# Optimization experiments

Measured on AMD Instinct MI355X. Metric: run time of the kernel, lower is better.

Reference implementation:

```python
import jax, jax.numpy as jnp
import numpy as np

B, D, H, NC = 4096, 128, 4, 10
HD = D // H
EPS = 1e-5


def _ln(x, g, b):
    m = jnp.mean(x, axis=-1, keepdims=True)
    v = jnp.var(x, axis=-1, keepdims=True)
    return (x - m) * jax.lax.rsqrt(v + EPS) * g + b


def _mlp(x, w1, b1, w2, b2):
    h = jax.nn.gelu(x @ w1.T + b1, approximate=False)  # nn.GELU default = exact erf
    return h @ w2.T + b2


def setup_inputs():
    key = jax.random.key(0)
    ks = iter(jax.random.split(key, 40))
    w = lambda *s: jax.random.normal(next(ks), s, dtype=jnp.float32) * 0.02
    inp = {
        'coords': jax.random.uniform(next(ks), (B, 2), dtype=jnp.float32),
        'labels': jax.random.randint(next(ks), (B,), 0, NC),
        'ce_w': w(D, 2), 'ce_b': w(D),
        'emb': w(NC, D),
        'sa_in_w': w(3 * D, D), 'sa_in_b': w(3 * D),
        'sa_out_w': w(D, D), 'sa_out_b': w(D),
        'n1_g': jnp.ones(D), 'n1_b': jnp.zeros(D),
        'm1_w1': w(4 * D, D), 'm1_b1': w(4 * D), 'm1_w2': w(D, 4 * D), 'm1_b2': w(D),
        'n2_g': jnp.ones(D), 'n2_b': jnp.zeros(D),
        'ca_in_w': w(3 * D, D), 'ca_in_b': w(3 * D),
        'ca_out_w': w(D, D), 'ca_out_b': w(D),
        'n3_g': jnp.ones(D), 'n3_b': jnp.zeros(D),
        'm2_w1': w(4 * D, D), 'm2_b1': w(4 * D), 'm2_w2': w(D, 4 * D), 'm2_b2': w(D),
        'n4_g': jnp.ones(D), 'n4_b': jnp.zeros(D),
        'fin_w': w(1, D), 'fin_b': w(1),
    }
    return inp


def reference(coords, labels, ce_w, ce_b, emb, sa_in_w, sa_in_b, sa_out_w, sa_out_b,
              n1_g, n1_b, m1_w1, m1_b1, m1_w2, m1_b2, n2_g, n2_b,
              ca_in_w, ca_in_b, ca_out_w, ca_out_b, n3_g, n3_b,
              m2_w1, m2_b1, m2_w2, m2_b2, n4_g, n4_b, fin_w, fin_b):
    # --- vectorized positional encoding (original loops over batch) ---
    div = 10000.0 ** (2.0 * jnp.arange(D // 2, dtype=jnp.float32) / D)  # [D/2]
    pe_sin = jnp.sin(coords[:, 0:1] / div)  # even slots
    pe_cos = jnp.cos(coords[:, 1:2] / div)  # odd slots
    pe = jnp.stack([pe_sin, pe_cos], axis=-1).reshape(B, D)

    x = coords @ ce_w.T + ce_b + pe  # [B, D]

    # --- self-attention: seq_len = B, batch = 1 (torch seq-first semantics) ---
    qkv = x @ sa_in_w.T + sa_in_b  # [B, 3D]
    q, k, v = jnp.split(qkv, 3, axis=-1)
    q = q.reshape(B, H, HD); k = k.reshape(B, H, HD); v = v.reshape(B, H, HD)
    scores = jnp.einsum('qhd,khd->hqk', q, k) / jnp.sqrt(jnp.float32(HD))  # [H,B,B]
    attn = jax.nn.softmax(scores, axis=-1)
    sa = jnp.einsum('hqk,khd->qhd', attn, v).reshape(B, D) @ sa_out_w.T + sa_out_b

    x = _ln(x + sa, n1_g, n1_b)
    x = _ln(x + _mlp(x, m1_w1, m1_b1, m1_w2, m1_b2), n2_g, n2_b)

    # --- cross-attention: per-sample q_len = kv_len = 1 -> softmax over a
    # single key is exactly 1, so output = out_proj(v_proj(label_emb)) ---
    lab = emb[labels]  # [B, D]
    wv = ca_in_w[2 * D:]; bv = ca_in_b[2 * D:]
    ca = (lab @ wv.T + bv) @ ca_out_w.T + ca_out_b

    x = _ln(x + ca, n3_g, n3_b)
    x = _ln(x + _mlp(x, m2_w1, m2_b1, m2_w2, m2_b2), n4_g, n4_b)

    return jax.nn.sigmoid(x @ fin_w.T + fin_b)  # [B, 1]
```

## Files before the change

### kernel.cpp

```cpp
#include <hip/hip_runtime.h>
#include <hip/hip_bf16.h>


typedef __bf16 bf16_t;
typedef __bf16 bf16x8 __attribute__((ext_vector_type(8)));
typedef __bf16 bf16x4 __attribute__((ext_vector_type(4)));
typedef __bf16 bf16x2 __attribute__((ext_vector_type(2)));
typedef float  f32x4  __attribute__((ext_vector_type(4)));
typedef float  f32x2  __attribute__((ext_vector_type(2)));

__device__ __forceinline__ f32x4 mfma16(bf16x8 a, bf16x8 b, f32x4 c) {
  return __builtin_amdgcn_mfma_f32_16x16x32_bf16(a, b, c, 0, 0, 0);
}

__global__ __launch_bounds__(256) void k_init(const float* __restrict__ coords,
                                              const float* __restrict__ ce_w,
                                              const float* __restrict__ ce_b,
                                              float* __restrict__ xf,
                                              bf16_t* __restrict__ xb,
                                              const float* __restrict__ s0,
                                              const float* __restrict__ s1,
                                              const float* __restrict__ s2,
                                              const float* __restrict__ s3,
                                              const float* __restrict__ s4,
                                              const float* __restrict__ s5,
                                              bf16_t* __restrict__ wdst,
                                              const float* __restrict__ emb,
                                              const float* __restrict__ wvp,
                                              const float* __restrict__ bvp,
                                              const float* __restrict__ cow,
                                              const float* __restrict__ cob,
                                              float* __restrict__ tab) {
  const int bid = blockIdx.x;
  const int tid = threadIdx.x;
  if (bid < 2048) {
    int row = bid * 2 + (tid >> 7);
    int d   = tid & 127;
    float c0 = coords[row * 2 + 0];
    float c1 = coords[row * 2 + 1];
    int   j  = d >> 1;
    float inv = exp2f(-0.20762050593045953f * (float)j);
    float pe  = (d & 1) ? cosf(c1 * inv) : sinf(c0 * inv);
    float x = c0 * ce_w[2 * d] + c1 * ce_w[2 * d + 1] + ce_b[d] + pe;
    xf[(size_t)row * 128 + d] = x;
    xb[(size_t)row * 128 + d] = (bf16_t)x;
  } else if (bid < 2368) {
    int i = (bid - 2048) * 256 + tid;
    const float* src; int off;
    if      (i < 12288) { src = s0; off = i; }
    else if (i < 16384) { src = s1; off = i - 12288; }
    else if (i < 32768) { src = s2; off = i - 16384; }
    else if (i < 49152) { src = s3; off = i - 32768; }
    else if (i < 65536) { src = s4; off = i - 49152; }
    else                { src = s5; off = i - 65536; }
    f32x4 v = *(const f32x4*)(src + (size_t)off * 4);
    bf16x4 o = {(bf16_t)v[0], (bf16_t)v[1], (bf16_t)v[2], (bf16_t)v[3]};
    *(bf16x4*)(wdst + (size_t)i * 4) = o;
  } else {
    __shared__ float embs[10][128];
    __shared__ float t1[10][128];
    for (int i = tid; i < 1280; i += 256) embs[i >> 7][i & 127] = emb[i];
    __syncthreads();
    for (int o = tid; o < 1280; o += 256) {
      int c = o >> 7, n = o & 127;
      float acc = bvp[n];
      const float* wr = wvp + n * 128;
      for (int k2 = 0; k2 < 128; k2++) acc += embs[c][k2] * wr[k2];
      t1[c][n] = acc;
    }
    __syncthreads();
    for (int o = tid; o < 1280; o += 256) {
      int c = o >> 7, dd = o & 127;
      float acc = cob[dd];
      const float* wr = cow + dd * 128;
      for (int n = 0; n < 128; n++) acc += t1[c][n] * wr[n];
      tab[o] = acc;
    }
  }
}

enum { EPI_BF16 = 1, EPI_GELU_BF16 = 2 };

template <int K, int EPI>
__global__ __launch_bounds__(256) void k_gemm(const bf16_t* __restrict__ X,
                                              const bf16_t* __restrict__ Wb,
                                              const float* __restrict__ bias,
                                              bf16_t* __restrict__ outB,
                                              bf16_t* __restrict__ vTout,
                                              int N) {
  const int tid  = threadIdx.x;
  const int lane = tid & 63;
  const int wv   = tid >> 6;
  const int l15  = lane & 15;
  const int quad = lane >> 4;
  const int xbase = blockIdx.x * 64 + (wv >> 1) * 32;
  const int wbase = blockIdx.y * 64 + (wv & 1) * 32;

  const bf16_t* wr0 = Wb + (size_t)(wbase + l15) * K + quad * 8;
  const bf16_t* xr0 = X  + (size_t)(xbase + l15) * K + quad * 8;

  f32x4 acc[2][2];
  const f32x4 zero4 = {0.f, 0.f, 0.f, 0.f};
  for (int i = 0; i < 2; i++)
    for (int t = 0; t < 2; t++) acc[i][t] = zero4;

#pragma unroll 4
  for (int kk = 0; kk < K; kk += 32) {
    bf16x8 a0 = *(const bf16x8*)(wr0 + kk);
    bf16x8 a1 = *(const bf16x8*)(wr0 + 16 * K + kk);
    bf16x8 b0 = *(const bf16x8*)(xr0 + kk);
    bf16x8 b1 = *(const bf16x8*)(xr0 + 16 * K + kk);
    acc[0][0] = mfma16(a0, b0, acc[0][0]);
    acc[0][1] = mfma16(a0, b1, acc[0][1]);
    acc[1][0] = mfma16(a1, b0, acc[1][0]);
    acc[1][1] = mfma16(a1, b1, acc[1][1]);
  }

  f32x4 bv[2];
  bv[0] = *(const f32x4*)(bias + wbase + quad * 4);
  bv[1] = *(const f32x4*)(bias + wbase + 16 + quad * 4);
#pragma unroll
  for (int t = 0; t < 2; t++) {
    int row = xbase + t * 16 + l15;
#pragma unroll
    for (int i = 0; i < 2; i++) {
      int col0 = wbase + i * 16 + quad * 4;
      f32x4 v = acc[i][t] + bv[i];
      if (EPI == EPI_GELU_BF16) {
#pragma unroll
        for (int r = 0; r < 4; r++)
          v[r] = 0.5f * v[r] * (1.0f + erff(v[r] * 0.70710678118654752f));
      }
      bf16x4 o = {(bf16_t)v[0], (bf16_t)v[1], (bf16_t)v[2], (bf16_t)v[3]};
      *(bf16x4*)(outB + (size_t)row * N + col0) = o;
      if (vTout && col0 >= 256) {
#pragma unroll
        for (int r = 0; r < 4; r++)
          vTout[(size_t)(col0 - 256 + r) * 4096 + row] = (bf16_t)v[r];
      }
    }
  }
}

__global__ __launch_bounds__(256, 4) void k_attn(const bf16_t* __restrict__ qkv,
                                                 const bf16_t* __restrict__ vT,
                                                 bf16_t* __restrict__ opart,
                                                 float* __restrict__ lpart) {
  __shared__ bf16_t kbuf[128][36];
  __shared__ bf16_t vbuf[32][136];
  __shared__ bf16_t pt[4][2][16][72];

  const int tid  = threadIdx.x;
  const int lane = tid & 63;
  const int wv   = tid >> 6;
  const int l15  = lane & 15;
  const int quad = lane >> 4;
  const int blk  = blockIdx.x;
  const int h    = blk & 3;
  const int ks   = (blk >> 2) & 7;
  const int qt   = (blk >> 5) * 4 + wv;
  const int q0   = qt * 32;
  const int kb   = ks * 512;
  const int task = (qt * 8 + ks) * 4 + h;

  bf16x8 qfA, qfB;
  {
    bf16x8 ra = *(const bf16x8*)(qkv + (size_t)(q0 + l15) * 384 + h * 32 + quad * 8);
    bf16x8 rb = *(const bf16x8*)(qkv + (size_t)(q0 + 16 + l15) * 384 + h * 32 + quad * 8);
#pragma unroll
    for (int j = 0; j < 8; j++) {
      qfA[j] = (bf16_t)((float)ra[j] * 0.17677669529663687f);
      qfB[j] = (bf16_t)((float)rb[j] * 0.17677669529663687f);
    }
  }

  const f32x4 zero4 = {0.f, 0.f, 0.f, 0.f};
  f32x4 oA0 = zero4, oA1 = zero4, oB0 = zero4, oB1 = zero4;
  float laccA = 0.f, laccB = 0.f;

  for (int kk = 0; kk < 512; kk += 128) {
    __syncthreads();
#pragma unroll
    for (int rep = 0; rep < 2; rep++) {
      int idx = rep * 256 + tid;
      int row = idx >> 2, seg = idx & 3;
      bf16x8 t8 = *(const bf16x8*)(qkv + (size_t)(kb + kk + row) * 384
                                   + 128 + h * 32 + seg * 8);
      *(bf16x8*)&kbuf[row][seg * 8] = t8;
      int dim = idx >> 4, vseg = idx & 15;
      bf16x8 v8 = *(const bf16x8*)(vT + (size_t)(h * 32 + dim) * 4096
                                   + kb + kk + vseg * 8);
      *(bf16x8*)&vbuf[dim][vseg * 8] = v8;
    }
    __syncthreads();

#pragma unroll
    for (int half = 0; half < 2; half++) {
      const int ko = half * 64;
      bf16x8 kf0 = *(const bf16x8*)&kbuf[ko + l15][quad * 8];
      bf16x8 kf1 = *(const bf16x8*)&kbuf[ko + 16 + l15][quad * 8];
      bf16x8 kf2 = *(const bf16x8*)&kbuf[ko + 32 + l15][quad * 8];
      bf16x8 kf3 = *(const bf16x8*)&kbuf[ko + 48 + l15][quad * 8];

      f32x4 sA[4], sB[4];
      sA[0] = mfma16(kf0, qfA, zero4);
      sA[1] = mfma16(kf1, qfA, zero4);
      sA[2] = mfma16(kf2, qfA, zero4);
      sA[3] = mfma16(kf3, qfA, zero4);
      sB[0] = mfma16(kf0, qfB, zero4);
      sB[1] = mfma16(kf1, qfB, zero4);
      sB[2] = mfma16(kf2, qfB, zero4);
      sB[3] = mfma16(kf3, qfB, zero4);

#pragma unroll
      for (int t = 0; t < 4; t++) {
        float a0 = __expf(sA[t][0]), a1 = __expf(sA[t][1]);
        float a2 = __expf(sA[t][2]), a3 = __expf(sA[t][3]);
        laccA += (a0 + a1) + (a2 + a3);
        bf16x4 pa = {(bf16_t)a0, (bf16_t)a1, (bf16_t)a2, (bf16_t)a3};
        *(bf16x4*)&pt[wv][0][l15][t * 16 + quad * 4] = pa;
        float b0 = __expf(sB[t][0]), b1 = __expf(sB[t][1]);
        float b2 = __expf(sB[t][2]), b3 = __expf(sB[t][3]);
        laccB += (b0 + b1) + (b2 + b3);
        bf16x4 pb = {(bf16_t)b0, (bf16_t)b1, (bf16_t)b2, (bf16_t)b3};
        *(bf16x4*)&pt[wv][1][l15][t * 16 + quad * 4] = pb;
      }

      bf16x8 pA0 = *(const bf16x8*)&pt[wv][0][l15][quad * 8];
      bf16x8 pA1 = *(const bf16x8*)&pt[wv][0][l15][32 + quad * 8];
      bf16x8 pB0 = *(const bf16x8*)&pt[wv][1][l15][quad * 8];
      bf16x8 pB1 = *(const bf16x8*)&pt[wv][1][l15][32 + quad * 8];

      bf16x8 v00 = *(const bf16x8*)&vbuf[l15][ko + quad * 8];
      bf16x8 v01 = *(const bf16x8*)&vbuf[16 + l15][ko + quad * 8];
      bf16x8 v10 = *(const bf16x8*)&vbuf[l15][ko + 32 + quad * 8];
      bf16x8 v11 = *(const bf16x8*)&vbuf[16 + l15][ko + 32 + quad * 8];

      oA0 = mfma16(pA0, v00, oA0);
      oA0 = mfma16(pA1, v10, oA0);
      oA1 = mfma16(pA0, v01, oA1);
      oA1 = mfma16(pA1, v11, oA1);
      oB0 = mfma16(pB0, v00, oB0);
      oB0 = mfma16(pB1, v10, oB0);
      oB1 = mfma16(pB0, v01, oB1);
      oB1 = mfma16(pB1, v11, oB1);
    }
  }

  laccA += __shfl_xor(laccA, 16, 64); laccA += __shfl_xor(laccA, 32, 64);
  laccB += __shfl_xor(laccB, 16, 64); laccB += __shfl_xor(laccB, 32, 64);
  if (quad == 0) {
    lpart[task * 32 + l15]      = laccA;
    lpart[task * 32 + 16 + l15] = laccB;
  }

  size_t ob = (size_t)task * 1024;
#pragma unroll
  for (int r = 0; r < 4; r++) {
    int qa = quad * 4 + r;
    opart[ob + qa * 32 + l15]             = (bf16_t)oA0[r];
    opart[ob + qa * 32 + 16 + l15]        = (bf16_t)oA1[r];
    opart[ob + (16 + qa) * 32 + l15]      = (bf16_t)oB0[r];
    opart[ob + (16 + qa) * 32 + 16 + l15] = (bf16_t)oB1[r];
  }
}

__global__ __launch_bounds__(256) void k_attn_fin(const bf16_t* __restrict__ opart,
                                                  const float* __restrict__ lpart,
                                                  bf16_t* __restrict__ attnb) {
  int idx = blockIdx.x * 256 + threadIdx.x;
  int d  = idx & 31;
  int q  = (idx >> 5) & 4095;
  int h  = idx >> 17;
  int qt = q >> 5, ql = q & 31;
  float O = 0.f, L = 0.f;
#pragma unroll
  for (int ks = 0; ks < 8; ks++) {
    int t = (qt * 8 + ks) * 4 + h;
    O += (float)opart[(size_t)t * 1024 + ql * 32 + d];
    L += lpart[t * 32 + ql];
  }
  attnb[(size_t)q * 128 + h * 32 + d] = (bf16_t)(O / L);
}

__global__ __launch_bounds__(512) void k_tail(
    const bf16_t* __restrict__ attnb, const float* __restrict__ xf,
    const bf16_t* __restrict__ wso, const float* __restrict__ bso,
    const float* __restrict__ n1g, const float* __restrict__ n1b,
    const bf16_t* __restrict__ w11, const float* __restrict__ b11,
    const bf16_t* __restrict__ w12, const float* __restrict__ b12,
    const float* __restrict__ n2g, const float* __restrict__ n2b,
    const int* __restrict__ labels, const float* __restrict__ tab,
    const float* __restrict__ n3g, const float* __restrict__ n3b,
    const bf16_t* __restrict__ w21, const float* __restrict__ b21,
    const bf16_t* __restrict__ w22, const float* __restrict__ b22,
    const float* __restrict__ n4g, const float* __restrict__ n4b,
    const float* __restrict__ fw, const float* __restrict__ fb,
    float* __restrict__ out) {
  __shared__ float  xs[16][132];
  __shared__ bf16_t xsb[16][136];
  __shared__ bf16_t hb[16][520];
  __shared__ float  red[2][16][8];

  const int tid  = threadIdx.x;
  const int lane = tid & 63;
  const int wv   = tid >> 6;
  const int l15  = lane & 15;
  const int quad = lane >> 4;
  const int row  = blockIdx.x * 16 + l15;
  const int cb1  = wv * 16;
  const int c1   = cb1 + quad * 4;
  const int cb4  = wv * 64;

  const f32x4 zero4 = {0.f, 0.f, 0.f, 0.f};

  {
    f32x4 acc = zero4;
    const bf16_t* br = attnb + (size_t)row * 128 + quad * 8;
    const bf16_t* ar = wso + (size_t)(cb1 + l15) * 128 + quad * 8;
#pragma unroll
    for (int kk = 0; kk < 128; kk += 32)
      acc = mfma16(*(const bf16x8*)(ar + kk), *(const bf16x8*)(br + kk), acc);

    f32x4 v = acc + *(const f32x4*)(bso + c1)
                  + *(const f32x4*)(xf + (size_t)row * 128 + c1);
    float s  = (v[0] + v[1]) + (v[2] + v[3]);
    float sq = (v[0]*v[0] + v[1]*v[1]) + (v[2]*v[2] + v[3]*v[3]);
    s  += __shfl_xor(s, 16, 64);  s  += __shfl_xor(s, 32, 64);
    sq += __shfl_xor(sq, 16, 64); sq += __shfl_xor(sq, 32, 64);
    if (quad == 0) { red[0][l15][wv] = s; red[1][l15][wv] = sq; }
    __syncthreads();
    float S = 0.f, SQ = 0.f;
#pragma unroll
    for (int w2 = 0; w2 < 8; w2++) { S += red[0][l15][w2]; SQ += red[1][l15][w2]; }
    float mean = S * (1.f / 128.f);
    float rstd = rsqrtf(SQ * (1.f / 128.f) - mean * mean + 1e-5f);
    f32x4 y = (v - mean) * rstd * (*(const f32x4*)(n1g + c1))
            + *(const f32x4*)(n1b + c1);
    *(f32x4*)&xs[l15][c1] = y;
    bf16x4 o = {(bf16_t)y[0], (bf16_t)y[1], (bf16_t)y[2], (bf16_t)y[3]};
    *(bf16x4*)&xsb[l15][c1] = o;
  }
  __syncthreads();

  {
    f32x4 au[4] = {zero4, zero4, zero4, zero4};
#pragma unroll
    for (int kk = 0; kk < 128; kk += 32) {
      bf16x8 bfr = *(const bf16x8*)&xsb[l15][kk + quad * 8];
#pragma unroll
      for (int i = 0; i < 4; i++) {
        bf16x8 a = *(const bf16x8*)(w11 + (size_t)(cb4 + i * 16 + l15) * 128
                                    + kk + quad * 8);
        au[i] = mfma16(a, bfr, au[i]);
      }
    }
#pragma unroll
    for (int i = 0; i < 4; i++) {
      int c = cb4 + i * 16 + quad * 4;
      f32x4 vv = au[i] + *(const f32x4*)(b11 + c);
#pragma unroll
      for (int r = 0; r < 4; r++)
        vv[r] = 0.5f * vv[r] * (1.0f + erff(vv[r] * 0.70710678118654752f));
      bf16x4 o = {(bf16_t)vv[0], (bf16_t)vv[1], (bf16_t)vv[2], (bf16_t)vv[3]};
      *(bf16x4*)&hb[l15][c] = o;
    }
  }
  __syncthreads();

  {
    f32x4 acc = zero4;
    const bf16_t* ar = w12 + (size_t)(cb1 + l15) * 512 + quad * 8;
#pragma unroll 4
    for (int kk = 0; kk < 512; kk += 32) {
      bf16x8 bfr = *(const bf16x8*)&hb[l15][kk + quad * 8];
      acc = mfma16(*(const bf16x8*)(ar + kk), bfr, acc);
    }
    f32x4 v = acc + *(const f32x4*)(b12 + c1) + *(const f32x4*)&xs[l15][c1];
    float s  = (v[0] + v[1]) + (v[2] + v[3]);
    float sq = (v[0]*v[0] + v[1]*v[1]) + (v[2]*v[2] + v[3]*v[3]);
    s  += __shfl_xor(s, 16, 64);  s  += __shfl_xor(s, 32, 64);
    sq += __shfl_xor(sq, 16, 64); sq += __shfl_xor(sq, 32, 64);
    if (quad == 0) { red[0][l15][wv] = s; red[1][l15][wv] = sq; }
    __syncthreads();
    float S = 0.f, SQ = 0.f;
#pragma unroll
    for (int w2 = 0; w2 < 8; w2++) { S += red[0][l15][w2]; SQ += red[1][l15][w2]; }
    float mean = S * (1.f / 128.f);
    float rstd = rsqrtf(SQ * (1.f / 128.f) - mean * mean + 1e-5f);
    int lab = labels[row];
    f32x4 y = (v - mean) * rstd * (*(const f32x4*)(n2g + c1))
            + *(const f32x4*)(n2b + c1)
            + *(const f32x4*)(tab + (size_t)lab * 128 + c1);
    float s3  = (y[0] + y[1]) + (y[2] + y[3]);
    float sq3 = (y[0]*y[0] + y[1]*y[1]) + (y[2]*y[2] + y[3]*y[3]);
    s3  += __shfl_xor(s3, 16, 64);  s3  += __shfl_xor(s3, 32, 64);
    sq3 += __shfl_xor(sq3, 16, 64); sq3 += __shfl_xor(sq3, 32, 64);
    __syncthreads();
    if (quad == 0) { red[0][l15][wv] = s3; red[1][l15][wv] = sq3; }
    __syncthreads();
    float S3 = 0.f, SQ3 = 0.f;
#pragma unroll
    for (int w2 = 0; w2 < 8; w2++) { S3 += red[0][l15][w2]; SQ3 += red[1][l15][w2]; }
    float mean3 = S3 * (1.f / 128.f);
    float rstd3 = rsqrtf(SQ3 * (1.f / 128.f) - mean3 * mean3 + 1e-5f);
    f32x4 y3 = (y - mean3) * rstd3 * (*(const f32x4*)(n3g + c1))
             + *(const f32x4*)(n3b + c1);
    *(f32x4*)&xs[l15][c1] = y3;
    bf16x4 o = {(bf16_t)y3[0], (bf16_t)y3[1], (bf16_t)y3[2], (bf16_t)y3[3]};
    *(bf16x4*)&xsb[l15][c1] = o;
  }
  __syncthreads();

  {
    f32x4 au[4] = {zero4, zero4, zero4, zero4};
#pragma unroll
    for (int kk = 0; kk < 128; kk += 32) {
      bf16x8 bfr = *(const bf16x8*)&xsb[l15][kk + quad * 8];
#pragma unroll
      for (int i = 0; i < 4; i++) {
        bf16x8 a = *(const bf16x8*)(w21 + (size_t)(cb4 + i * 16 + l15) * 128
                                    + kk + quad * 8);
        au[i] = mfma16(a, bfr, au[i]);
      }
    }
#pragma unroll
    for (int i = 0; i < 4; i++) {
      int c = cb4 + i * 16 + quad * 4;
      f32x4 vv = au[i] + *(const f32x4*)(b21 + c);
#pragma unroll
      for (int r = 0; r < 4; r++)
        vv[r] = 0.5f * vv[r] * (1.0f + erff(vv[r] * 0.70710678118654752f));
      bf16x4 o = {(bf16_t)vv[0], (bf16_t)vv[1], (bf16_t)vv[2], (bf16_t)vv[3]};
      *(bf16x4*)&hb[l15][c] = o;
    }
  }
  __syncthreads();

  {
    f32x4 acc = zero4;
    const bf16_t* ar = w22 + (size_t)(cb1 + l15) * 512 + quad * 8;
#pragma unroll 4
    for (int kk = 0; kk < 512; kk += 32) {
      bf16x8 bfr = *(const bf16x8*)&hb[l15][kk + quad * 8];
      acc = mfma16(*(const bf16x8*)(ar + kk), bfr, acc);
    }
    f32x4 v = acc + *(const f32x4*)(b22 + c1) + *(const f32x4*)&xs[l15][c1];
    float s  = (v[0] + v[1]) + (v[2] + v[3]);
    float sq = (v[0]*v[0] + v[1]*v[1]) + (v[2]*v[2] + v[3]*v[3]);
    s  += __shfl_xor(s, 16, 64);  s  += __shfl_xor(s, 32, 64);
    sq += __shfl_xor(sq, 16, 64); sq += __shfl_xor(sq, 32, 64);
    if (quad == 0) { red[0][l15][wv] = s; red[1][l15][wv] = sq; }
    __syncthreads();
    float S = 0.f, SQ = 0.f;
#pragma unroll
    for (int w2 = 0; w2 < 8; w2++) { S += red[0][l15][w2]; SQ += red[1][l15][w2]; }
    float mean = S * (1.f / 128.f);
    float rstd = rsqrtf(SQ * (1.f / 128.f) - mean * mean + 1e-5f);
    f32x4 y = (v - mean) * rstd * (*(const f32x4*)(n4g + c1))
            + *(const f32x4*)(n4b + c1);
    f32x4 fwv = *(const f32x4*)(fw + c1);
    float dot = (y[0]*fwv[0] + y[1]*fwv[1]) + (y[2]*fwv[2] + y[3]*fwv[3]);
    dot += __shfl_xor(dot, 16, 64); dot += __shfl_xor(dot, 32, 64);
    __syncthreads();
    if (quad == 0) red[0][l15][wv] = dot;
    __syncthreads();
    if (wv == 0 && quad == 0) {
      float logit = fb[0];
#pragma unroll
      for (int w2 = 0; w2 < 8; w2++) logit += red[0][l15][w2];
      out[row] = 1.0f / (1.0f + expf(-logit));
    }
  }
}

extern "C" void kernel_launch(void* const* d_in, const int* in_sizes, int n_in,
                              void* d_out, int out_size, void* d_ws, size_t ws_size,
                              hipStream_t stream) {
  const float* coords  = (const float*)d_in[0];
  const int*   labels  = (const int*)d_in[1];
  const float* ce_w    = (const float*)d_in[2];
  const float* ce_b    = (const float*)d_in[3];
  const float* emb     = (const float*)d_in[4];
  const float* sa_in_w = (const float*)d_in[5];
  const float* sa_in_b = (const float*)d_in[6];
  const float* sa_out_w= (const float*)d_in[7];
  const float* sa_out_b= (const float*)d_in[8];
  const float* n1_g    = (const float*)d_in[9];
  const float* n1_b    = (const float*)d_in[10];
  const float* m1_w1   = (const float*)d_in[11];
  const float* m1_b1   = (const float*)d_in[12];
  const float* m1_w2   = (const float*)d_in[13];
  const float* m1_b2   = (const float*)d_in[14];
  const float* n2_g    = (const float*)d_in[15];
  const float* n2_b    = (const float*)d_in[16];
  const float* ca_in_w = (const float*)d_in[17];
  const float* ca_in_b = (const float*)d_in[18];
  const float* ca_out_w= (const float*)d_in[19];
  const float* ca_out_b= (const float*)d_in[20];
  const float* n3_g    = (const float*)d_in[21];
  const float* n3_b    = (const float*)d_in[22];
  const float* m2_w1   = (const float*)d_in[23];
  const float* m2_b1   = (const float*)d_in[24];
  const float* m2_w2   = (const float*)d_in[25];
  const float* m2_b2   = (const float*)d_in[26];
  const float* n4_g    = (const float*)d_in[27];
  const float* n4_b    = (const float*)d_in[28];
  const float* fin_w   = (const float*)d_in[29];
  const float* fin_b   = (const float*)d_in[30];
  float* outp = (float*)d_out;

  char* w = (char*)d_ws;
  float*  xf    = (float*)(w);
  float*  tab   = (float*)(w + 2097152);
  bf16_t* wsb   = (bf16_t*)(w + 2105344);
  bf16_t* xb    = (bf16_t*)(w + 2760704);
  bf16_t* attnb = (bf16_t*)(w + 3809280);
  bf16_t* qkvb  = (bf16_t*)(w + 4857856);
  bf16_t* vT    = (bf16_t*)(w + 8003584);
  bf16_t* opart = (bf16_t*)(w + 9052160);
  float*  lpart = (float*)(w + 17440768);

  bf16_t* w_sain  = wsb;
  bf16_t* w_saout = wsb + 49152;
  bf16_t* w_m1w1  = wsb + 65536;
  bf16_t* w_m1w2  = wsb + 131072;
  bf16_t* w_m2w1  = wsb + 196608;
  bf16_t* w_m2w2  = wsb + 262144;

  k_init<<<2369, 256, 0, stream>>>(coords, ce_w, ce_b, xf, xb,
                                   sa_in_w, sa_out_w, m1_w1, m1_w2, m2_w1, m2_w2,
                                   wsb, emb, ca_in_w + 256 * 128, ca_in_b + 256,
                                   ca_out_w, ca_out_b, tab);
  k_gemm<128, EPI_BF16><<<dim3(64, 6), 256, 0, stream>>>(xb, w_sain, sa_in_b,
                                                         qkvb, vT, 384);
  k_attn<<<1024, 256, 0, stream>>>(qkvb, vT, opart, lpart);
  k_attn_fin<<<2048, 256, 0, stream>>>(opart, lpart, attnb);
  k_tail<<<256, 512, 0, stream>>>(attnb, xf,
                                  w_saout, sa_out_b, n1_g, n1_b,
                                  w_m1w1, m1_b1, w_m1w2, m1_b2, n2_g, n2_b,
                                  labels, tab, n3_g, n3_b,
                                  w_m2w1, m2_b1, w_m2w2, m2_b2, n4_g, n4_b,
                                  fin_w, fin_b, outp);

  (void)in_sizes; (void)n_in; (void)out_size; (void)ws_size;
}
```

Baseline: 192.6 us.

## Fuse all stages into one cooperative persistent kernel with grid syncs

Merges the init, QKV GEMM, attention, attention-finalize and tail kernels into a single cooperative kernel of 256 blocks x 512 threads, separated by grid.sync barriers. The attention-finalize step now runs inside the tail phase, so the bf16 attention output no longer goes through global memory. The aim is to remove launch overheads and inter-kernel gaps. In exchange, attention runs on far fewer resident waves (two task iterations per 4-wave group instead of 1024 independent blocks), which may lower latency hiding, and each grid-wide barrier adds its own cost.

```diff
diff --git a/kernel.cpp b/kernel.cpp
--- a/kernel.cpp
+++ b/kernel.cpp
@@ -1,475 +1,470 @@
 #include <hip/hip_runtime.h>
 #include <hip/hip_bf16.h>
-
+#include <hip/hip_cooperative_groups.h>
+
+
+namespace cg = cooperative_groups;
 
 typedef __bf16 bf16_t;
 typedef __bf16 bf16x8 __attribute__((ext_vector_type(8)));
 typedef __bf16 bf16x4 __attribute__((ext_vector_type(4)));
-typedef __bf16 bf16x2 __attribute__((ext_vector_type(2)));
 typedef float  f32x4  __attribute__((ext_vector_type(4)));
-typedef float  f32x2  __attribute__((ext_vector_type(2)));
 
 __device__ __forceinline__ f32x4 mfma16(bf16x8 a, bf16x8 b, f32x4 c) {
   return __builtin_amdgcn_mfma_f32_16x16x32_bf16(a, b, c, 0, 0, 0);
 }
 
-__global__ __launch_bounds__(256) void k_init(const float* __restrict__ coords,
-                                              const float* __restrict__ ce_w,
-                                              const float* __restrict__ ce_b,
-                                              float* __restrict__ xf,
-                                              bf16_t* __restrict__ xb,
-                                              const float* __restrict__ s0,
-                                              const float* __restrict__ s1,
-                                              const float* __restrict__ s2,
-                                              const float* __restrict__ s3,
-                                              const float* __restrict__ s4,
-                                              const float* __restrict__ s5,
-                                              bf16_t* __restrict__ wdst,
-                                              const float* __restrict__ emb,
-                                              const float* __restrict__ wvp,
-                                              const float* __restrict__ bvp,
-                                              const float* __restrict__ cow,
-                                              const float* __restrict__ cob,
-                                              float* __restrict__ tab) {
-  const int bid = blockIdx.x;
-  const int tid = threadIdx.x;
-  if (bid < 2048) {
-    int row = bid * 2 + (tid >> 7);
-    int d   = tid & 127;
-    float c0 = coords[row * 2 + 0];
-    float c1 = coords[row * 2 + 1];
-    int   j  = d >> 1;
-    float inv = exp2f(-0.20762050593045953f * (float)j);
-    float pe  = (d & 1) ? cosf(c1 * inv) : sinf(c0 * inv);
-    float x = c0 * ce_w[2 * d] + c1 * ce_w[2 * d + 1] + ce_b[d] + pe;
-    xf[(size_t)row * 128 + d] = x;
-    xb[(size_t)row * 128 + d] = (bf16_t)x;
-  } else if (bid < 2368) {
-    int i = (bid - 2048) * 256 + tid;
-    const float* src; int off;
-    if      (i < 12288) { src = s0; off = i; }
-    else if (i < 16384) { src = s1; off = i - 12288; }
-    else if (i < 32768) { src = s2; off = i - 16384; }
-    else if (i < 49152) { src = s3; off = i - 32768; }
-    else if (i < 65536) { src = s4; off = i - 49152; }
-    else                { src = s5; off = i - 65536; }
-    f32x4 v = *(const f32x4*)(src + (size_t)off * 4);
-    bf16x4 o = {(bf16_t)v[0], (bf16_t)v[1], (bf16_t)v[2], (bf16_t)v[3]};
-    *(bf16x4*)(wdst + (size_t)i * 4) = o;
-  } else {
-    __shared__ float embs[10][128];
-    __shared__ float t1[10][128];
-    for (int i = tid; i < 1280; i += 256) embs[i >> 7][i & 127] = emb[i];
-    __syncthreads();
-    for (int o = tid; o < 1280; o += 256) {
-      int c = o >> 7, n = o & 127;
-      float acc = bvp[n];
-      const float* wr = wvp + n * 128;
-      for (int k2 = 0; k2 < 128; k2++) acc += embs[c][k2] * wr[k2];
-      t1[c][n] = acc;
-    }
-    __syncthreads();
-    for (int o = tid; o < 1280; o += 256) {
-      int c = o >> 7, dd = o & 127;
-      float acc = cob[dd];
-      const float* wr = cow + dd * 128;
-      for (int n = 0; n < 128; n++) acc += t1[c][n] * wr[n];
-      tab[o] = acc;
-    }
-  }
-}
-
-enum { EPI_BF16 = 1, EPI_GELU_BF16 = 2 };
-
-template <int K, int EPI>
-__global__ __launch_bounds__(256) void k_gemm(const bf16_t* __restrict__ X,
-                                              const bf16_t* __restrict__ Wb,
-                                              const float* __restrict__ bias,
-                                              bf16_t* __restrict__ outB,
-                                              bf16_t* __restrict__ vTout,
-                                              int N) {
+struct P {
+  const float* coords; const int* labels;
+  const float* ce_w;   const float* ce_b;
+  const float* sa_in_b; const float* sa_out_b;
+  const float* n1g; const float* n1b;
+  const float* m1_b1; const float* m1_b2;
+  const float* n2g; const float* n2b;
+  const float* n3g; const float* n3b;
+  const float* m2_b1; const float* m2_b2;
+  const float* n4g; const float* n4b;
+  const float* fin_w; const float* fin_b;
+  const float* s0; const float* s1; const float* s2;
+  const float* s3; const float* s4; const float* s5;
+  const float* emb; const float* wvp; const float* bvp;
+  const float* cow; const float* cob;
+  float* xf; float* tab; bf16_t* wsb; bf16_t* xb;
+  bf16_t* qkvb; bf16_t* vT; bf16_t* opart; float* lpart;
+  const bf16_t* w_sain; const bf16_t* w_saout;
+  const bf16_t* w_m1w1; const bf16_t* w_m1w2;
+  const bf16_t* w_m2w1; const bf16_t* w_m2w2;
+  float* out;
+};
+
+#define SM_KBUF(g)  ((g) * 9216)
+#define SM_VBUF(g)  (18432 + (g) * 8704)
+#define SM_PT(wv)   (35840 + (wv) * 4608)
+
+__global__ __launch_bounds__(512, 2) void k_fused(P p) {
+  cg::grid_group grid = cg::this_grid();
+  __shared__ char smem[74240] __attribute__((aligned(16)));
+
+  const int b    = blockIdx.x;
   const int tid  = threadIdx.x;
   const int lane = tid & 63;
   const int wv   = tid >> 6;
   const int l15  = lane & 15;
   const int quad = lane >> 4;
-  const int xbase = blockIdx.x * 64 + (wv >> 1) * 32;
-  const int wbase = blockIdx.y * 64 + (wv & 1) * 32;
-
-  const bf16_t* wr0 = Wb + (size_t)(wbase + l15) * K + quad * 8;
-  const bf16_t* xr0 = X  + (size_t)(xbase + l15) * K + quad * 8;
-
-  f32x4 acc[2][2];
   const f32x4 zero4 = {0.f, 0.f, 0.f, 0.f};
-  for (int i = 0; i < 2; i++)
-    for (int t = 0; t < 2; t++) acc[i][t] = zero4;
-
+
+  {
+    int c = b * 512 + tid;
+    int row = c >> 5, d0 = (c & 31) * 4;
+    float c0 = p.coords[row * 2 + 0];
+    float c1 = p.coords[row * 2 + 1];
+    f32x4 xv; bf16x4 xo;
+#pragma unroll
+    for (int r = 0; r < 4; r++) {
+      int d = d0 + r, j = d >> 1;
+      float inv = exp2f(-0.20762050593045953f * (float)j);
+      float pe  = (d & 1) ? cosf(c1 * inv) : sinf(c0 * inv);
+      float x = c0 * p.ce_w[2 * d] + c1 * p.ce_w[2 * d + 1] + p.ce_b[d] + pe;
+      xv[r] = x; xo[r] = (bf16_t)x;
+    }
+    *(f32x4*)(p.xf + (size_t)row * 128 + d0) = xv;
+    *(bf16x4*)(p.xb + (size_t)row * 128 + d0) = xo;
+
+    if (c < 81920) {
+      const float* src; int off;
+      if      (c < 12288) { src = p.s0; off = c; }
+      else if (c < 16384) { src = p.s1; off = c - 12288; }
+      else if (c < 32768) { src = p.s2; off = c - 16384; }
+      else if (c < 49152) { src = p.s3; off = c - 32768; }
+      else if (c < 65536) { src = p.s4; off = c - 49152; }
+      else                { src = p.s5; off = c - 65536; }
+      f32x4 v = *(const f32x4*)(src + (size_t)off * 4);
+      bf16x4 o = {(bf16_t)v[0], (bf16_t)v[1], (bf16_t)v[2], (bf16_t)v[3]};
+      *(bf16x4*)(p.wsb + (size_t)c * 4) = o;
+    }
+
+    if (b == 255) {
+      float (*embs)[128] = (float(*)[128])smem;
+      float (*t1)[128]   = (float(*)[128])(smem + 5120);
+      for (int i = tid; i < 1280; i += 512) embs[i >> 7][i & 127] = p.emb[i];
+      __syncthreads();
+      for (int o = tid; o < 1280; o += 512) {
+        int cc = o >> 7, n = o & 127;
+        float acc = p.bvp[n];
+        const float* wr = p.wvp + n * 128;
+        for (int k2 = 0; k2 < 128; k2++) acc += embs[cc][k2] * wr[k2];
+        t1[cc][n] = acc;
+      }
+      __syncthreads();
+      for (int o = tid; o < 1280; o += 512) {
+        int cc = o >> 7, dd = o & 127;
+        float acc = p.cob[dd];
+        const float* wr = p.cow + dd * 128;
+        for (int n = 0; n < 128; n++) acc += t1[cc][n] * wr[n];
+        p.tab[o] = acc;
+      }
+    }
+  }
+  __threadfence();
+  grid.sync();
+
+  {
+    int W = b * 8 + wv;
+    if (W < 1536) {
+      int rt = W / 12, ct = W - rt * 12;
+      int row0 = rt * 32, col0 = ct * 32;
+      const bf16_t* wr0 = p.w_sain + (size_t)(col0 + l15) * 128 + quad * 8;
+      const bf16_t* xr0 = p.xb + (size_t)(row0 + l15) * 128 + quad * 8;
+      f32x4 acc[2][2];
+      for (int i = 0; i < 2; i++)
+        for (int t = 0; t < 2; t++) acc[i][t] = zero4;
+#pragma unroll
+      for (int kk = 0; kk < 128; kk += 32) {
+        bf16x8 a0 = *(const bf16x8*)(wr0 + kk);
+        bf16x8 a1 = *(const bf16x8*)(wr0 + 16 * 128 + kk);
+        bf16x8 b0 = *(const bf16x8*)(xr0 + kk);
+        bf16x8 b1 = *(const bf16x8*)(xr0 + 16 * 128 + kk);
+        acc[0][0] = mfma16(a0, b0, acc[0][0]);
+        acc[0][1] = mfma16(a0, b1, acc[0][1]);
+        acc[1][0] = mfma16(a1, b0, acc[1][0]);
+        acc[1][1] = mfma16(a1, b1, acc[1][1]);
+      }
+      f32x4 bv[2];
+      bv[0] = *(const f32x4*)(p.sa_in_b + col0 + quad * 4);
+      bv[1] = *(const f32x4*)(p.sa_in_b + col0 + 16 + quad * 4);
+#pragma unroll
+      for (int t = 0; t < 2; t++) {
+        int row = row0 + t * 16 + l15;
+#pragma unroll
+        for (int i = 0; i < 2; i++) {
+          int colb = col0 + i * 16 + quad * 4;
+          f32x4 v = acc[i][t] + bv[i];
+          bf16x4 o = {(bf16_t)v[0], (bf16_t)v[1], (bf16_t)v[2], (bf16_t)v[3]};
+          *(bf16x4*)(p.qkvb + (size_t)row * 384 + colb) = o;
+          if (colb >= 256) {
+#pragma unroll
+            for (int r = 0; r < 4; r++)
+              p.vT[(size_t)(colb - 256 + r) * 4096 + row] = (bf16_t)v[r];
+          }
+        }
+      }
+    }
+  }
+  __threadfence();
+  grid.sync();
+
+  {
+    const int g    = wv >> 2;
+    const int wl   = wv & 3;
+    const int gtid = wl * 64 + lane;
+    bf16_t (*kbuf)[36]      = (bf16_t(*)[36])(smem + SM_KBUF(g));
+    bf16_t (*vbuf)[136]     = (bf16_t(*)[136])(smem + SM_VBUF(g));
+    bf16_t (*ptw)[16][72]   = (bf16_t(*)[16][72])(smem + SM_PT(wv));
+
+    for (int j = 0; j < 2; j++) {
+      int orig = b * 4 + g * 2 + j;
+      int h  = orig & 3;
+      int ks = (orig >> 2) & 7;
+      int qt = (orig >> 5) * 4 + wl;
+      int q0 = qt * 32;
+      int kb = ks * 512;
+      int task = (qt * 8 + ks) * 4 + h;
+
+      bf16x8 qfA, qfB;
+      {
+        bf16x8 ra = *(const bf16x8*)(p.qkvb + (size_t)(q0 + l15) * 384 + h * 32 + quad * 8);
+        bf16x8 rb = *(const bf16x8*)(p.qkvb + (size_t)(q0 + 16 + l15) * 384 + h * 32 + quad * 8);
+#pragma unroll
+        for (int jj = 0; jj < 8; jj++) {
+          qfA[jj] = (bf16_t)((float)ra[jj] * 0.17677669529663687f);
+          qfB[jj] = (bf16_t)((float)rb[jj] * 0.17677669529663687f);
+        }
+      }
+
+      f32x4 oA0 = zero4, oA1 = zero4, oB0 = zero4, oB1 = zero4;
+      float laccA = 0.f, laccB = 0.f;
+
+      for (int kk = 0; kk < 512; kk += 128) {
+        __syncthreads();
+#pragma unroll
+        for (int rep = 0; rep < 2; rep++) {
+          int idx = rep * 256 + gtid;
+          int krow = idx >> 2, seg = idx & 3;
+          bf16x8 t8 = *(const bf16x8*)(p.qkvb + (size_t)(kb + kk + krow) * 384
+                                       + 128 + h * 32 + seg * 8);
+          *(bf16x8*)&kbuf[krow][seg * 8] = t8;
+          int dim = idx >> 4, vseg = idx & 15;
+          bf16x8 v8 = *(const bf16x8*)(p.vT + (size_t)(h * 32 + dim) * 4096
+                                       + kb + kk + vseg * 8);
+          *(bf16x8*)&vbuf[dim][vseg * 8] = v8;
+        }
+        __syncthreads();
+
+#pragma unroll
+        for (int half = 0; half < 2; half++) {
+          const int ko = half * 64;
+          bf16x8 kf0 = *(const bf16x8*)&kbuf[ko + l15][quad * 8];
+          bf16x8 kf1 = *(const bf16x8*)&kbuf[ko + 16 + l15][quad * 8];
+          bf16x8 kf2 = *(const bf16x8*)&kbuf[ko + 32 + l15][quad * 8];
+          bf16x8 kf3 = *(const bf16x8*)&kbuf[ko + 48 + l15][quad * 8];
+
+          f32x4 sA[4], sB[4];
+          sA[0] = mfma16(kf0, qfA, zero4);
+          sA[1] = mfma16(kf1, qfA, zero4);
+          sA[2] = mfma16(kf2, qfA, zero4);
+          sA[3] = mfma16(kf3, qfA, zero4);
+          sB[0] = mfma16(kf0, qfB, zero4);
+          sB[1] = mfma16(kf1, qfB, zero4);
+          sB[2] = mfma16(kf2, qfB, zero4);
+          sB[3] = mfma16(kf3, qfB, zero4);
+
+#pragma unroll
+          for (int t = 0; t < 4; t++) {
+            float a0 = __expf(sA[t][0]), a1 = __expf(sA[t][1]);
+            float a2 = __expf(sA[t][2]), a3 = __expf(sA[t][3]);
+            laccA += (a0 + a1) + (a2 + a3);
+            bf16x4 pa = {(bf16_t)a0, (bf16_t)a1, (bf16_t)a2, (bf16_t)a3};
+            *(bf16x4*)&ptw[0][l15][t * 16 + quad * 4] = pa;
+            float b0 = __expf(sB[t][0]), b1 = __expf(sB[t][1]);
+            float b2 = __expf(sB[t][2]), b3 = __expf(sB[t][3]);
+            laccB += (b0 + b1) + (b2 + b3);
+            bf16x4 pb = {(bf16_t)b0, (bf16_t)b1, (bf16_t)b2, (bf16_t)b3};
+            *(bf16x4*)&ptw[1][l15][t * 16 + quad * 4] = pb;
+          }
+
+          bf16x8 pA0 = *(const bf16x8*)&ptw[0][l15][quad * 8];
+          bf16x8 pA1 = *(const bf16x8*)&ptw[0][l15][32 + quad * 8];
+          bf16x8 pB0 = *(const bf16x8*)&ptw[1][l15][quad * 8];
+          bf16x8 pB1 = *(const bf16x8*)&ptw[1][l15][32 + quad * 8];
+
+          bf16x8 v00 = *(const bf16x8*)&vbuf[l15][ko + quad * 8];
+          bf16x8 v01 = *(const bf16x8*)&vbuf[16 + l15][ko + quad * 8];
+          bf16x8 v10 = *(const bf16x8*)&vbuf[l15][ko + 32 + quad * 8];
+          bf16x8 v11 = *(const bf16x8*)&vbuf[16 + l15][ko + 32 + quad * 8];
+
+          oA0 = mfma16(pA0, v00, oA0);
+          oA0 = mfma16(pA1, v10, oA0);
+          oA1 = mfma16(pA0, v01, oA1);
+          oA1 = mfma16(pA1, v11, oA1);
+          oB0 = mfma16(pB0, v00, oB0);
+          oB0 = mfma16(pB1, v10, oB0);
+          oB1 = mfma16(pB0, v01, oB1);
+          oB1 = mfma16(pB1, v11, oB1);
+        }
+      }
+
+      laccA += __shfl_xor(laccA, 16, 64); laccA += __shfl_xor(laccA, 32, 64);
+      laccB += __shfl_xor(laccB, 16, 64); laccB += __shfl_xor(laccB, 32, 64);
+      if (quad == 0) {
+        p.lpart[task * 32 + l15]      = laccA;
+        p.lpart[task * 32 + 16 + l15] = laccB;
+      }
+      size_t ob = (size_t)task * 1024;
+#pragma unroll
+      for (int r = 0; r < 4; r++) {
+        int qa = quad * 4 + r;
+        p.opart[ob + qa * 32 + l15]             = (bf16_t)oA0[r];
+        p.opart[ob + qa * 32 + 16 + l15]        = (bf16_t)oA1[r];
+        p.opart[ob + (16 + qa) * 32 + l15]      = (bf16_t)oB0[r];
+        p.opart[ob + (16 + qa) * 32 + 16 + l15] = (bf16_t)oB1[r];
+      }
+    }
+  }
+  __threadfence();
+  grid.sync();
+
+  {
+    float  (*xs)[132]    = (float(*)[132])(smem);
+    bf16_t (*xsb)[136]   = (bf16_t(*)[136])(smem + 8448);
+    bf16_t (*att)[136]   = (bf16_t(*)[136])(smem + 12800);
+    bf16_t (*hb)[520]    = (bf16_t(*)[520])(smem + 17152);
+    float  (*red)[16][8] = (float(*)[16][8])(smem + 33792);
+    float  (*Ls)[4]      = (float(*)[4])(smem + 34816);
+
+    const int row = b * 16 + l15;
+    const int cb1 = wv * 16;
+    const int c1  = cb1 + quad * 4;
+    const int cb4 = wv * 64;
+
+    if (tid < 64) {
+      int rr = tid >> 2, hh = tid & 3;
+      int q = b * 16 + rr, qt = q >> 5, ql = q & 31;
+      float L = 0.f;
+#pragma unroll
+      for (int ks = 0; ks < 8; ks++) L += p.lpart[((qt * 8 + ks) * 4 + hh) * 32 + ql];
+      Ls[rr][hh] = L;
+    }
+    __syncthreads();
+#pragma unroll
+    for (int r = 0; r < 4; r++) {
+      int idx = r * 512 + tid;
+      int rr = idx >> 7, d = idx & 127, hh = d >> 5, dd = d & 31;
+      int q = b * 16 + rr, qt = q >> 5, ql = q & 31;
+      float O = 0.f;
+#pragma unroll
+      for (int ks = 0; ks < 8; ks++)
+        O += (float)p.opart[(size_t)((qt * 8 + ks) * 4 + hh) * 1024 + ql * 32 + dd];
+      att[rr][d] = (bf16_t)(O / Ls[rr][hh]);
+    }
+    __syncthreads();
+
+    {
+      f32x4 acc = zero4;
+      const bf16_t* ar = p.w_saout + (size_t)(cb1 + l15) * 128 + quad * 8;
+#pragma unroll
+      for (int kk = 0; kk < 128; kk += 32) {
+        bf16x8 bfr = *(const bf16x8*)&att[l15][kk + quad * 8];
+        acc = mfma16(*(const bf16x8*)(ar + kk), bfr, acc);
+      }
+      f32x4 v = acc + *(const f32x4*)(p.sa_out_b + c1)
+                    + *(const f32x4*)(p.xf + (size_t)row * 128 + c1);
+      float s  = (v[0] + v[1]) + (v[2] + v[3]);
+      float sq = (v[0]*v[0] + v[1]*v[1]) + (v[2]*v[2] + v[3]*v[3]);
+      s  += __shfl_xor(s, 16, 64);  s  += __shfl_xor(s, 32, 64);
+      sq += __shfl_xor(sq, 16, 64); sq += __shfl_xor(sq, 32, 64);
+      if (quad == 0) { red[0][l15][wv] = s; red[1][l15][wv] = sq; }
+      __syncthreads();
+      float S = 0.f, SQ = 0.f;
+#pragma unroll
+      for (int w2 = 0; w2 < 8; w2++) { S += red[0][l15][w2]; SQ += red[1][l15][w2]; }
+      float mean = S * (1.f / 128.f);
+      float rstd = rsqrtf(SQ * (1.f / 128.f) - mean * mean + 1e-5f);
+      f32x4 y = (v - mean) * rstd * (*(const f32x4*)(p.n1g + c1))
+              + *(const f32x4*)(p.n1b + c1);
+      *(f32x4*)&xs[l15][c1] = y;
+      bf16x4 o = {(bf16_t)y[0], (bf16_t)y[1], (bf16_t)y[2], (bf16_t)y[3]};
+      *(bf16x4*)&xsb[l15][c1] = o;
+    }
+    __syncthreads();
+
+    {
+      f32x4 au[4] = {zero4, zero4, zero4, zero4};
+#pragma unroll
+      for (int kk = 0; kk < 128; kk += 32) {
+        bf16x8 bfr = *(const bf16x8*)&xsb[l15][kk + quad * 8];
+#pragma unroll
+        for (int i = 0; i < 4; i++) {
+          bf16x8 a = *(const bf16x8*)(p.w_m1w1 + (size_t)(cb4 + i * 16 + l15) * 128
+                                      + kk + quad * 8);
+          au[i] = mfma16(a, bfr, au[i]);
+        }
+      }
+#pragma unroll
+      for (int i = 0; i < 4; i++) {
+        int c = cb4 + i * 16 + quad * 4;
+        f32x4 vv = au[i] + *(const f32x4*)(p.m1_b1 + c);
+#pragma unroll
+        for (int r = 0; r < 4; r++)
+          vv[r] = 0.5f * vv[r] * (1.0f + erff(vv[r] * 0.70710678118654752f));
+        bf16x4 o = {(bf16_t)vv[0], (bf16_t)vv[1], (bf16_t)vv[2], (bf16_t)vv[3]};
+        *(bf16x4*)&hb[l15][c] = o;
+      }
+    }
+    __syncthreads();
+
+    {
+      f32x4 acc = zero4;
+      const bf16_t* ar = p.w_m1w2 + (size_t)(cb1 + l15) * 512 + quad * 8;
 #pragma unroll 4
-  for (int kk = 0; kk < K; kk += 32) {
-    bf16x8 a0 = *(const bf16x8*)(wr0 + kk);
-    bf16x8 a1 = *(const bf16x8*)(wr0 + 16 * K + kk);
-    bf16x8 b0 = *(const bf16x8*)(xr0 + kk);
-    bf16x8 b1 = *(const bf16x8*)(xr0 + 16 * K + kk);
-    acc[0][0] = mfma16(a0, b0, acc[0][0]);
-    acc[0][1] = mfma16(a0, b1, acc[0][1]);
-    acc[1][0] = mfma16(a1, b0, acc[1][0]);
-    acc[1][1] = mfma16(a1, b1, acc[1][1]);
-  }
-
-  f32x4 bv[2];
-  bv[0] = *(const f32x4*)(bias + wbase + quad * 4);
-  bv[1] = *(const f32x4*)(bias + wbase + 16 + quad * 4);
-#pragma unroll
-  for (int t = 0; t < 2; t++) {
-    int row = xbase + t * 16 + l15;
-#pragma unroll
-    for (int i = 0; i < 2; i++) {
-      int col0 = wbase + i * 16 + quad * 4;
-      f32x4 v = acc[i][t] + bv[i];
-      if (EPI == EPI_GELU_BF16) {
+      for (int kk = 0; kk < 512; kk += 32) {
+        bf16x8 bfr = *(const bf16x8*)&hb[l15][kk + quad * 8];
+        acc = mfma16(*(const bf16x8*)(ar + kk), bfr, acc);
+      }
+      f32x4 v = acc + *(const f32x4*)(p.m1_b2 + c1) + *(const f32x4*)&xs[l15][c1];
+      float s  = (v[0] + v[1]) + (v[2] + v[3]);
+      float sq = (v[0]*v[0] + v[1]*v[1]) + (v[2]*v[2] + v[3]*v[3]);
+      s  += __shfl_xor(s, 16, 64);  s  += __shfl_xor(s, 32, 64);
+      sq += __shfl_xor(sq, 16, 64); sq += __shfl_xor(sq, 32, 64);
+      if (quad == 0) { red[0][l15][wv] = s; red[1][l15][wv] = sq; }
+      __syncthreads();
+      float S = 0.f, SQ = 0.f;
+#pragma unroll
+      for (int w2 = 0; w2 < 8; w2++) { S += red[0][l15][w2]; SQ += red[1][l15][w2]; }
+      float mean = S * (1.f / 128.f);
+      float rstd = rsqrtf(SQ * (1.f / 128.f) - mean * mean + 1e-5f);
+      int lab = p.labels[row];
+      f32x4 y = (v - mean) * rstd * (*(const f32x4*)(p.n2g + c1))
+              + *(const f32x4*)(p.n2b + c1)
+              + *(const f32x4*)(p.tab + (size_t)lab * 128 + c1);
+      float s3  = (y[0] + y[1]) + (y[2] + y[3]);
+      float sq3 = (y[0]*y[0] + y[1]*y[1]) + (y[2]*y[2] + y[3]*y[3]);
+      s3  += __shfl_xor(s3, 16, 64);  s3  += __shfl_xor(s3, 32, 64);
+      sq3 += __shfl_xor(sq3, 16, 64); sq3 += __shfl_xor(sq3, 32, 64);
+      __syncthreads();
+      if (quad == 0) { red[0][l15][wv] = s3; red[1][l15][wv] = sq3; }
+      __syncthreads();
+      float S3 = 0.f, SQ3 = 0.f;
+#pragma unroll
+      for (int w2 = 0; w2 < 8; w2++) { S3 += red[0][l15][w2]; SQ3 += red[1][l15][w2]; }
+      float mean3 = S3 * (1.f / 128.f);
+      float rstd3 = rsqrtf(SQ3 * (1.f / 128.f) - mean3 * mean3 + 1e-5f);
+      f32x4 y3 = (y - mean3) * rstd3 * (*(const f32x4*)(p.n3g + c1))
+               + *(const f32x4*)(p.n3b + c1);
+      *(f32x4*)&xs[l15][c1] = y3;
+      bf16x4 o = {(bf16_t)y3[0], (bf16_t)y3[1], (bf16_t)y3[2], (bf16_t)y3[3]};
+      *(bf16x4*)&xsb[l15][c1] = o;
+    }
+    __syncthreads();
+
+    {
+      f32x4 au[4] = {zero4, zero4, zero4, zero4};
+#pragma unroll
+      for (int kk = 0; kk < 128; kk += 32) {
+        bf16x8 bfr = *(const bf16x8*)&xsb[l15][kk + quad * 8];
+#pragma unroll
+        for (int i = 0; i < 4; i++) {
+          bf16x8 a = *(const bf16x8*)(p.w_m2w1 + (size_t)(cb4 + i * 16 + l15) * 128
+                                      + kk + quad * 8);
+          au[i] = mfma16(a, bfr, au[i]);
+        }
+      }
+#pragma unroll
+      for (int i = 0; i < 4; i++) {
+        int c = cb4 + i * 16 + quad * 4;
+        f32x4 vv = au[i] + *(const f32x4*)(p.m2_b1 + c);
 #pragma unroll
         for (int r = 0; r < 4; r++)
-          v[r] = 0.5f * v[r] * (1.0f + erff(v[r] * 0.70710678118654752f));
-      }
-      bf16x4 o = {(bf16_t)v[0], (bf16_t)v[1], (bf16_t)v[2], (bf16_t)v[3]};
-      *(bf16x4*)(outB + (size_t)row * N + col0) = o;
-      if (vTout && col0 >= 256) {
-#pragma unroll
-        for (int r = 0; r < 4; r++)
-          vTout[(size_t)(col0 - 256 + r) * 4096 + row] = (bf16_t)v[r];
-      }
-    }
-  }
-}
-
-__global__ __launch_bounds__(256, 4) void k_attn(const bf16_t* __restrict__ qkv,
-                                                 const bf16_t* __restrict__ vT,
-                                                 bf16_t* __restrict__ opart,
-                                                 float* __restrict__ lpart) {
-  __shared__ bf16_t kbuf[128][36];
-  __shared__ bf16_t vbuf[32][136];
-  __shared__ bf16_t pt[4][2][16][72];
-
-  const int tid  = threadIdx.x;
-  const int lane = tid & 63;
-  const int wv   = tid >> 6;
-  const int l15  = lane & 15;
-  const int quad = lane >> 4;
-  const int blk  = blockIdx.x;
-  const int h    = blk & 3;
-  const int ks   = (blk >> 2) & 7;
-  const int qt   = (blk >> 5) * 4 + wv;
-  const int q0   = qt * 32;
-  const int kb   = ks * 512;
-  const int task = (qt * 8 + ks) * 4 + h;
-
-  bf16x8 qfA, qfB;
-  {
-    bf16x8 ra = *(const bf16x8*)(qkv + (size_t)(q0 + l15) * 384 + h * 32 + quad * 8);
-    bf16x8 rb = *(const bf16x8*)(qkv + (size_t)(q0 + 16 + l15) * 384 + h * 32 + quad * 8);
-#pragma unroll
-    for (int j = 0; j < 8; j++) {
-      qfA[j] = (bf16_t)((float)ra[j] * 0.17677669529663687f);
-      qfB[j] = (bf16_t)((float)rb[j] * 0.17677669529663687f);
-    }
-  }
-
-  const f32x4 zero4 = {0.f, 0.f, 0.f, 0.f};
-  f32x4 oA0 = zero4, oA1 = zero4, oB0 = zero4, oB1 = zero4;
-  float laccA = 0.f, laccB = 0.f;
-
-  for (int kk = 0; kk < 512; kk += 128) {
+          vv[r] = 0.5f * vv[r] * (1.0f + erff(vv[r] * 0.70710678118654752f));
+        bf16x4 o = {(bf16_t)vv[0], (bf16_t)vv[1], (bf16_t)vv[2], (bf16_t)vv[3]};
+        *(bf16x4*)&hb[l15][c] = o;
+      }
+    }
     __syncthreads();
-#pragma unroll
-    for (int rep = 0; rep < 2; rep++) {
-      int idx = rep * 256 + tid;
-      int row = idx >> 2, seg = idx & 3;
-      bf16x8 t8 = *(const bf16x8*)(qkv + (size_t)(kb + kk + row) * 384
-                                   + 128 + h * 32 + seg * 8);
-      *(bf16x8*)&kbuf[row][seg * 8] = t8;
-      int dim = idx >> 4, vseg = idx & 15;
-      bf16x8 v8 = *(const bf16x8*)(vT + (size_t)(h * 32 + dim) * 4096
-                                   + kb + kk + vseg * 8);
-      *(bf16x8*)&vbuf[dim][vseg * 8] = v8;
-    }
-    __syncthreads();
-
-#pragma unroll
-    for (int half = 0; half < 2; half++) {
-      const int ko = half * 64;
-      bf16x8 kf0 = *(const bf16x8*)&kbuf[ko + l15][quad * 8];
-      bf16x8 kf1 = *(const bf16x8*)&kbuf[ko + 16 + l15][quad * 8];
-      bf16x8 kf2 = *(const bf16x8*)&kbuf[ko + 32 + l15][quad * 8];
-      bf16x8 kf3 = *(const bf16x8*)&kbuf[ko + 48 + l15][quad * 8];
-
-      f32x4 sA[4], sB[4];
-      sA[0] = mfma16(kf0, qfA, zero4);
-      sA[1] = mfma16(kf1, qfA, zero4);
-      sA[2] = mfma16(kf2, qfA, zero4);
-      sA[3] = mfma16(kf3, qfA, zero4);
-      sB[0] = mfma16(kf0, qfB, zero4);
-      sB[1] = mfma16(kf1, qfB, zero4);
-      sB[2] = mfma16(kf2, qfB, zero4);
-      sB[3] = mfma16(kf3, qfB, zero4);
-
-#pragma unroll
-      for (int t = 0; t < 4; t++) {
-        float a0 = __expf(sA[t][0]), a1 = __expf(sA[t][1]);
-        float a2 = __expf(sA[t][2]), a3 = __expf(sA[t][3]);
-        laccA += (a0 + a1) + (a2 + a3);
-        bf16x4 pa = {(bf16_t)a0, (bf16_t)a1, (bf16_t)a2, (bf16_t)a3};
-        *(bf16x4*)&pt[wv][0][l15][t * 16 + quad * 4] = pa;
-        float b0 = __expf(sB[t][0]), b1 = __expf(sB[t][1]);
-        float b2 = __expf(sB[t][2]), b3 = __expf(sB[t][3]);
-        laccB += (b0 + b1) + (b2 + b3);
-        bf16x4 pb = {(bf16_t)b0, (bf16_t)b1, (bf16_t)b2, (bf16_t)b3};
-        *(bf16x4*)&pt[wv][1][l15][t * 16 + quad * 4] = pb;
-      }
-
-      bf16x8 pA0 = *(const bf16x8*)&pt[wv][0][l15][quad * 8];
-      bf16x8 pA1 = *(const bf16x8*)&pt[wv][0][l15][32 + quad * 8];
-      bf16x8 pB0 = *(const bf16x8*)&pt[wv][1][l15][quad * 8];
-      bf16x8 pB1 = *(const bf16x8*)&pt[wv][1][l15][32 + quad * 8];
-
-      bf16x8 v00 = *(const bf16x8*)&vbuf[l15][ko + quad * 8];
-      bf16x8 v01 = *(const bf16x8*)&vbuf[16 + l15][ko + quad * 8];
-      bf16x8 v10 = *(const bf16x8*)&vbuf[l15][ko + 32 + quad * 8];
-      bf16x8 v11 = *(const bf16x8*)&vbuf[16 + l15][ko + 32 + quad * 8];
-
-      oA0 = mfma16(pA0, v00, oA0);
-      oA0 = mfma16(pA1, v10, oA0);
-      oA1 = mfma16(pA0, v01, oA1);
-      oA1 = mfma16(pA1, v11, oA1);
-      oB0 = mfma16(pB0, v00, oB0);
-      oB0 = mfma16(pB1, v10, oB0);
-      oB1 = mfma16(pB0, v01, oB1);
-      oB1 = mfma16(pB1, v11, oB1);
-    }
-  }
-
-  laccA += __shfl_xor(laccA, 16, 64); laccA += __shfl_xor(laccA, 32, 64);
-  laccB += __shfl_xor(laccB, 16, 64); laccB += __shfl_xor(laccB, 32, 64);
-  if (quad == 0) {
-    lpart[task * 32 + l15]      = laccA;
-    lpart[task * 32 + 16 + l15] = laccB;
-  }
-
-  size_t ob = (size_t)task * 1024;
-#pragma unroll
-  for (int r = 0; r < 4; r++) {
-    int qa = quad * 4 + r;
-    opart[ob + qa * 32 + l15]             = (bf16_t)oA0[r];
-    opart[ob + qa * 32 + 16 + l15]        = (bf16_t)oA1[r];
-    opart[ob + (16 + qa) * 32 + l15]      = (bf16_t)oB0[r];
-    opart[ob + (16 + qa) * 32 + 16 + l15] = (bf16_t)oB1[r];
-  }
-}
-
-__global__ __launch_bounds__(256) void k_attn_fin(const bf16_t* __restrict__ opart,
-                                                  const float* __restrict__ lpart,
-                                                  bf16_t* __restrict__ attnb) {
-  int idx = blockIdx.x * 256 + threadIdx.x;
-  int d  = idx & 31;
-  int q  = (idx >> 5) & 4095;
-  int h  = idx >> 17;
-  int qt = q >> 5, ql = q & 31;
-  float O = 0.f, L = 0.f;
-#pragma unroll
-  for (int ks = 0; ks < 8; ks++) {
-    int t = (qt * 8 + ks) * 4 + h;
-    O += (float)opart[(size_t)t * 1024 + ql * 32 + d];
-    L += lpart[t * 32 + ql];
-  }
-  attnb[(size_t)q * 128 + h * 32 + d] = (bf16_t)(O / L);
-}
-
-__global__ __launch_bounds__(512) void k_tail(
-    const bf16_t* __restrict__ attnb, const float* __restrict__ xf,
-    const bf16_t* __restrict__ wso, const float* __restrict__ bso,
-    const float* __restrict__ n1g, const float* __restrict__ n1b,
-    const bf16_t* __restrict__ w11, const float* __restrict__ b11,
-    const bf16_t* __restrict__ w12, const float* __restrict__ b12,
-    const float* __restrict__ n2g, const float* __restrict__ n2b,
-    const int* __restrict__ labels, const float* __restrict__ tab,
-    const float* __restrict__ n3g, const float* __restrict__ n3b,
-    const bf16_t* __restrict__ w21, const float* __restrict__ b21,
-    const bf16_t* __restrict__ w22, const float* __restrict__ b22,
-    const float* __restrict__ n4g, const float* __restrict__ n4b,
-    const float* __restrict__ fw, const float* __restrict__ fb,
-    float* __restrict__ out) {
-  __shared__ float  xs[16][132];
-  __shared__ bf16_t xsb[16][136];
-  __shared__ bf16_t hb[16][520];
-  __shared__ float  red[2][16][8];
-
-  const int tid  = threadIdx.x;
-  const int lane = tid & 63;
-  const int wv   = tid >> 6;
-  const int l15  = lane & 15;
-  const int quad = lane >> 4;
-  const int row  = blockIdx.x * 16 + l15;
-  const int cb1  = wv * 16;
-  const int c1   = cb1 + quad * 4;
-  const int cb4  = wv * 64;
-
-  const f32x4 zero4 = {0.f, 0.f, 0.f, 0.f};
-
-  {
-    f32x4 acc = zero4;
-    const bf16_t* br = attnb + (size_t)row * 128 + quad * 8;
-    const bf16_t* ar = wso + (size_t)(cb1 + l15) * 128 + quad * 8;
-#pragma unroll
-    for (int kk = 0; kk < 128; kk += 32)
-      acc = mfma16(*(const bf16x8*)(ar + kk), *(const bf16x8*)(br + kk), acc);
-
-    f32x4 v = acc + *(const f32x4*)(bso + c1)
-                  + *(const f32x4*)(xf + (size_t)row * 128 + c1);
-    float s  = (v[0] + v[1]) + (v[2] + v[3]);
-    float sq = (v[0]*v[0] + v[1]*v[1]) + (v[2]*v[2] + v[3]*v[3]);
-    s  += __shfl_xor(s, 16, 64);  s  += __shfl_xor(s, 32, 64);
-    sq += __shfl_xor(sq, 16, 64); sq += __shfl_xor(sq, 32, 64);
-    if (quad == 0) { red[0][l15][wv] = s; red[1][l15][wv] = sq; }
-    __syncthreads();
-    float S = 0.f, SQ = 0.f;
-#pragma unroll
-    for (int w2 = 0; w2 < 8; w2++) { S += red[0][l15][w2]; SQ += red[1][l15][w2]; }
-    float mean = S * (1.f / 128.f);
-    float rstd = rsqrtf(SQ * (1.f / 128.f) - mean * mean + 1e-5f);
-    f32x4 y = (v - mean) * rstd * (*(const f32x4*)(n1g + c1))
-            + *(const f32x4*)(n1b + c1);
-    *(f32x4*)&xs[l15][c1] = y;
-    bf16x4 o = {(bf16_t)y[0], (bf16_t)y[1], (bf16_t)y[2], (bf16_t)y[3]};
-    *(bf16x4*)&xsb[l15][c1] = o;
-  }
-  __syncthreads();
-
-  {
-    f32x4 au[4] = {zero4, zero4, zero4, zero4};
-#pragma unroll
-    for (int kk = 0; kk < 128; kk += 32) {
-      bf16x8 bfr = *(const bf16x8*)&xsb[l15][kk + quad * 8];
-#pragma unroll
-      for (int i = 0; i < 4; i++) {
-        bf16x8 a = *(const bf16x8*)(w11 + (size_t)(cb4 + i * 16 + l15) * 128
-                                    + kk + quad * 8);
-        au[i] = mfma16(a, bfr, au[i]);
-      }
-    }
-#pragma unroll
-    for (int i = 0; i < 4; i++) {
-      int c = cb4 + i * 16 + quad * 4;
-      f32x4 vv = au[i] + *(const f32x4*)(b11 + c);
-#pragma unroll
-      for (int r = 0; r < 4; r++)
-        vv[r] = 0.5f * vv[r] * (1.0f + erff(vv[r] * 0.70710678118654752f));
-      bf16x4 o = {(bf16_t)vv[0], (bf16_t)vv[1], (bf16_t)vv[2], (bf16_t)vv[3]};
-      *(bf16x4*)&hb[l15][c] = o;
-    }
-  }
-  __syncthreads();
-
-  {
-    f32x4 acc = zero4;
-    const bf16_t* ar = w12 + (size_t)(cb1 + l15) * 512 + quad * 8;
+
+    {
+      f32x4 acc = zero4;
+      const bf16_t* ar = p.w_m2w2 + (size_t)(cb1 + l15) * 512 + quad * 8;
 #pragma unroll 4
-    for (int kk = 0; kk < 512; kk += 32) {
-      bf16x8 bfr = *(const bf16x8*)&hb[l15][kk + quad * 8];
-      acc = mfma16(*(const bf16x8*)(ar + kk), bfr, acc);
-    }
-    f32x4 v = acc + *(const f32x4*)(b12 + c1) + *(const f32x4*)&xs[l15][c1];
-    float s  = (v[0] + v[1]) + (v[2] + v[3]);
-    float sq = (v[0]*v[0] + v[1]*v[1]) + (v[2]*v[2] + v[3]*v[3]);
-    s  += __shfl_xor(s, 16, 64);  s  += __shfl_xor(s, 32, 64);
-    sq += __shfl_xor(sq, 16, 64); sq += __shfl_xor(sq, 32, 64);
-    if (quad == 0) { red[0][l15][wv] = s; red[1][l15][wv] = sq; }
-    __syncthreads();
-    float S = 0.f, SQ = 0.f;
-#pragma unroll
-    for (int w2 = 0; w2 < 8; w2++) { S += red[0][l15][w2]; SQ += red[1][l15][w2]; }
-    float mean = S * (1.f / 128.f);
-    float rstd = rsqrtf(SQ * (1.f / 128.f) - mean * mean + 1e-5f);
-    int lab = labels[row];
-    f32x4 y = (v - mean) * rstd * (*(const f32x4*)(n2g + c1))
-            + *(const f32x4*)(n2b + c1)
-            + *(const f32x4*)(tab + (size_t)lab * 128 + c1);
-    float s3  = (y[0] + y[1]) + (y[2] + y[3]);
-    float sq3 = (y[0]*y[0] + y[1]*y[1]) + (y[2]*y[2] + y[3]*y[3]);
-    s3  += __shfl_xor(s3, 16, 64);  s3  += __shfl_xor(s3, 32, 64);
-    sq3 += __shfl_xor(sq3, 16, 64); sq3 += __shfl_xor(sq3, 32, 64);
-    __syncthreads();
-    if (quad == 0) { red[0][l15][wv] = s3; red[1][l15][wv] = sq3; }
-    __syncthreads();
-    float S3 = 0.f, SQ3 = 0.f;
-#pragma unroll
-    for (int w2 = 0; w2 < 8; w2++) { S3 += red[0][l15][w2]; SQ3 += red[1][l15][w2]; }
-    float mean3 = S3 * (1.f / 128.f);
-    float rstd3 = rsqrtf(SQ3 * (1.f / 128.f) - mean3 * mean3 + 1e-5f);
-    f32x4 y3 = (y - mean3) * rstd3 * (*(const f32x4*)(n3g + c1))
-             + *(const f32x4*)(n3b + c1);
-    *(f32x4*)&xs[l15][c1] = y3;
-    bf16x4 o = {(bf16_t)y3[0], (bf16_t)y3[1], (bf16_t)y3[2], (bf16_t)y3[3]};
-    *(bf16x4*)&xsb[l15][c1] = o;
-  }
-  __syncthreads();
-
-  {
-    f32x4 au[4] = {zero4, zero4, zero4, zero4};
-#pragma unroll
-    for (int kk = 0; kk < 128; kk += 32) {
-      bf16x8 bfr = *(const bf16x8*)&xsb[l15][kk + quad * 8];
-#pragma unroll
-      for (int i = 0; i < 4; i++) {
-        bf16x8 a = *(const bf16x8*)(w21 + (size_t)(cb4 + i * 16 + l15) * 128
-                                    + kk + quad * 8);
-        au[i] = mfma16(a, bfr, au[i]);
-      }
-    }
-#pragma unroll
-    for (int i = 0; i < 4; i++) {
-      int c = cb4 + i * 16 + quad * 4;
-      f32x4 vv = au[i] + *(const f32x4*)(b21 + c);
-#pragma unroll
-      for (int r = 0; r < 4; r++)
-        vv[r] = 0.5f * vv[r] * (1.0f + erff(vv[r] * 0.70710678118654752f));
-      bf16x4 o = {(bf16_t)vv[0], (bf16_t)vv[1], (bf16_t)vv[2], (bf16_t)vv[3]};
-      *(bf16x4*)&hb[l15][c] = o;
-    }
-  }
-  __syncthreads();
-
-  {
-    f32x4 acc = zero4;
-    const bf16_t* ar = w22 + (size_t)(cb1 + l15) * 512 + quad * 8;
-#pragma unroll 4
-    for (int kk = 0; kk < 512; kk += 32) {
-      bf16x8 bfr = *(const bf16x8*)&hb[l15][kk + quad * 8];
-      acc = mfma16(*(const bf16x8*)(ar + kk), bfr, acc);
-    }
-    f32x4 v = acc + *(const f32x4*)(b22 + c1) + *(const f32x4*)&xs[l15][c1];
-    float s  = (v[0] + v[1]) + (v[2] + v[3]);
-    float sq = (v[0]*v[0] + v[1]*v[1]) + (v[2]*v[2] + v[3]*v[3]);
-    s  += __shfl_xor(s, 16, 64);  s  += __shfl_xor(s, 32, 64);
-    sq += __shfl_xor(sq, 16, 64); sq += __shfl_xor(sq, 32, 64);
-    if (quad == 0) { red[0][l15][wv] = s; red[1][l15][wv] = sq; }
-    __syncthreads();
-    float S = 0.f, SQ = 0.f;
-#pragma unroll
-    for (int w2 = 0; w2 < 8; w2++) { S += red[0][l15][w2]; SQ += red[1][l15][w2]; }
-    float mean = S * (1.f / 128.f);
-    float rstd = rsqrtf(SQ * (1.f / 128.f) - mean * mean + 1e-5f);
-    f32x4 y = (v - mean) * rstd * (*(const f32x4*)(n4g + c1))
-            + *(const f32x4*)(n4b + c1);
-    f32x4 fwv = *(const f32x4*)(fw + c1);
-    float dot = (y[0]*fwv[0] + y[1]*fwv[1]) + (y[2]*fwv[2] + y[3]*fwv[3]);
-    dot += __shfl_xor(dot, 16, 64); dot += __shfl_xor(dot, 32, 64);
-    __syncthreads();
-    if (quad == 0) red[0][l15][wv] = dot;
-    __syncthreads();
-    if (wv == 0 && quad == 0) {
-      float logit = fb[0];
-#pragma unroll
-      for (int w2 = 0; w2 < 8; w2++) logit += red[0][l15][w2];
-      out[row] = 1.0f / (1.0f + expf(-logit));
+      for (int kk = 0; kk < 512; kk += 32) {
+        bf16x8 bfr = *(const bf16x8*)&hb[l15][kk + quad * 8];
+        acc = mfma16(*(const bf16x8*)(ar + kk), bfr, acc);
+      }
+      f32x4 v = acc + *(const f32x4*)(p.m2_b2 + c1) + *(const f32x4*)&xs[l15][c1];
+      float s  = (v[0] + v[1]) + (v[2] + v[3]);
+      float sq = (v[0]*v[0] + v[1]*v[1]) + (v[2]*v[2] + v[3]*v[3]);
+      s  += __shfl_xor(s, 16, 64);  s  += __shfl_xor(s, 32, 64);
+      sq += __shfl_xor(sq, 16, 64); sq += __shfl_xor(sq, 32, 64);
+      if (quad == 0) { red[0][l15][wv] = s; red[1][l15][wv] = sq; }
+      __syncthreads();
+      float S = 0.f, SQ = 0.f;
+#pragma unroll
+      for (int w2 = 0; w2 < 8; w2++) { S += red[0][l15][w2]; SQ += red[1][l15][w2]; }
+      float mean = S * (1.f / 128.f);
+      float rstd = rsqrtf(SQ * (1.f / 128.f) - mean * mean + 1e-5f);
+      f32x4 y = (v - mean) * rstd * (*(const f32x4*)(p.n4g + c1))
+              + *(const f32x4*)(p.n4b + c1);
+      f32x4 fwv = *(const f32x4*)(p.fin_w + c1);
+      float dot = (y[0]*fwv[0] + y[1]*fwv[1]) + (y[2]*fwv[2] + y[3]*fwv[3]);
+      dot += __shfl_xor(dot, 16, 64); dot += __shfl_xor(dot, 32, 64);
+      __syncthreads();
+      if (quad == 0) red[0][l15][wv] = dot;
+      __syncthreads();
+      if (wv == 0 && quad == 0) {
+        float logit = p.fin_b[0];
+#pragma unroll
+        for (int w2 = 0; w2 < 8; w2++) logit += red[0][l15][w2];
+        p.out[row] = 1.0f / (1.0f + expf(-logit));
+      }
     }
   }
 }
@@ -508,40 +503,45 @@
   const float* n4_b    = (const float*)d_in[28];
   const float* fin_w   = (const float*)d_in[29];
   const float* fin_b   = (const float*)d_in[30];
-  float* outp = (float*)d_out;
 
   char* w = (char*)d_ws;
-  float*  xf    = (float*)(w);
-  float*  tab   = (float*)(w + 2097152);
-  bf16_t* wsb   = (bf16_t*)(w + 2105344);
-  bf16_t* xb    = (bf16_t*)(w + 2760704);
-  bf16_t* attnb = (bf16_t*)(w + 3809280);
-  bf16_t* qkvb  = (bf16_t*)(w + 4857856);
-  bf16_t* vT    = (bf16_t*)(w + 8003584);
-  bf16_t* opart = (bf16_t*)(w + 9052160);
-  float*  lpart = (float*)(w + 17440768);
-
-  bf16_t* w_sain  = wsb;
-  bf16_t* w_saout = wsb + 49152;
-  bf16_t* w_m1w1  = wsb + 65536;
-  bf16_t* w_m1w2  = wsb + 131072;
-  bf16_t* w_m2w1  = wsb + 196608;
-  bf16_t* w_m2w2  = wsb + 262144;
-
-  k_init<<<2369, 256, 0, stream>>>(coords, ce_w, ce_b, xf, xb,
-                                   sa_in_w, sa_out_w, m1_w1, m1_w2, m2_w1, m2_w2,
-                                   wsb, emb, ca_in_w + 256 * 128, ca_in_b + 256,
-                                   ca_out_w, ca_out_b, tab);
-  k_gemm<128, EPI_BF16><<<dim3(64, 6), 256, 0, stream>>>(xb, w_sain, sa_in_b,
-                                                         qkvb, vT, 384);
-  k_attn<<<1024, 256, 0, stream>>>(qkvb, vT, opart, lpart);
-  k_attn_fin<<<2048, 256, 0, stream>>>(opart, lpart, attnb);
-  k_tail<<<256, 512, 0, stream>>>(attnb, xf,
-                                  w_saout, sa_out_b, n1_g, n1_b,
-                                  w_m1w1, m1_b1, w_m1w2, m1_b2, n2_g, n2_b,
-                                  labels, tab, n3_g, n3_b,
-                                  w_m2w1, m2_b1, w_m2w2, m2_b2, n4_g, n4_b,
-                                  fin_w, fin_b, outp);
+  P prm;
+  prm.coords = coords; prm.labels = labels;
+  prm.ce_w = ce_w; prm.ce_b = ce_b;
+  prm.sa_in_b = sa_in_b; prm.sa_out_b = sa_out_b;
+  prm.n1g = n1_g; prm.n1b = n1_b;
+  prm.m1_b1 = m1_b1; prm.m1_b2 = m1_b2;
+  prm.n2g = n2_g; prm.n2b = n2_b;
+  prm.n3g = n3_g; prm.n3b = n3_b;
+  prm.m2_b1 = m2_b1; prm.m2_b2 = m2_b2;
+  prm.n4g = n4_g; prm.n4b = n4_b;
+  prm.fin_w = fin_w; prm.fin_b = fin_b;
+  prm.s0 = sa_in_w; prm.s1 = sa_out_w; prm.s2 = m1_w1;
+  prm.s3 = m1_w2;   prm.s4 = m2_w1;    prm.s5 = m2_w2;
+  prm.emb = emb;
+  prm.wvp = ca_in_w + 256 * 128; prm.bvp = ca_in_b + 256;
+  prm.cow = ca_out_w; prm.cob = ca_out_b;
+
+  prm.xf    = (float*)(w);
+  prm.tab   = (float*)(w + 2097152);
+  prm.wsb   = (bf16_t*)(w + 2105344);
+  prm.xb    = (bf16_t*)(w + 2760704);
+  prm.qkvb  = (bf16_t*)(w + 4857856);
+  prm.vT    = (bf16_t*)(w + 8003584);
+  prm.opart = (bf16_t*)(w + 9052160);
+  prm.lpart = (float*)(w + 17440768);
+
+  prm.w_sain  = prm.wsb;
+  prm.w_saout = prm.wsb + 49152;
+  prm.w_m1w1  = prm.wsb + 65536;
+  prm.w_m1w2  = prm.wsb + 131072;
+  prm.w_m2w1  = prm.wsb + 196608;
+  prm.w_m2w2  = prm.wsb + 262144;
+  prm.out = (float*)d_out;
+
+  void* args[] = {(void*)&prm};
+  hipLaunchCooperativeKernel((const void*)k_fused, dim3(256), dim3(512),
+                             args, 0, stream);
 
   (void)in_sizes; (void)n_in; (void)out_size; (void)ws_size;
 }
```

Result: slower. 505.3 us (+162.4%).
